# Optimization experiments

Hardware: AMD Instinct MI355X
Metric: run time of the kernel (lower is better)

## Reference

```python
import jax, jax.numpy as jnp
import numpy as np

SEQ, B, N, H, OUT, K, L = 32, 1024, 19, 128, 1, 2, 2


def setup_inputs() -> dict:
    key = jax.random.key(0)
    ks = jax.random.split(key, 16)
    s = lambda i, shape, scale=1.0: (jax.random.normal(ks[i], shape, jnp.float32) * scale)
    return {
        "inputs": s(0, (SEQ, B, N, OUT)),
        "initial_hidden_state": s(1, (L, B, N * H)),
        "support": s(2, (N, N)) * (1.0 / np.sqrt(N)),
        "W_gate0": s(3, (3 * (OUT + H), 2 * H)) * 0.05,
        "b_gate0": s(4, (2 * H,)) * 0.05,
        "W_cand0": s(5, (3 * (OUT + H), H)) * 0.05,
        "b_cand0": s(6, (H,)) * 0.05,
        "W_gate1": s(7, (3 * (H + H), 2 * H)) * 0.05,
        "b_gate1": s(8, (2 * H,)) * 0.05,
        "W_cand1": s(9, (3 * (H + H), H)) * 0.05,
        "b_cand1": s(10, (H,)) * 0.05,
        "W_proj": s(11, (H, OUT)) * 0.05,
        "b_proj": s(12, (OUT,)) * 0.05,
    }


def reference(inputs, initial_hidden_state, support, W_gate0, b_gate0, W_cand0,
              b_cand0, W_gate1, b_gate1, W_cand1, b_cand1, W_proj, b_proj):
    seq_len, batch = inputs.shape[0], inputs.shape[1]
    h0 = initial_hidden_state.reshape(L, batch, N, H)

    def gconv(x, W, b):
        # Chebyshev diffusion: x0, T1=S@x0, T2=2*S@T1-x0 (K=2, 1 support)
        x0 = x
        x1 = jnp.einsum('mn,bnf->bmf', support, x0)
        feats = [x0, x1]
        for _ in range(K - 1):
            x2 = 2.0 * jnp.einsum('mn,bnf->bmf', support, x1) - x0
            feats.append(x2)
            x0, x1 = x1, x2
        X = jnp.concatenate(feats, axis=-1)  # (B, N, F*num_matrices)
        return jnp.einsum('bnf,fo->bno', X, W) + b

    def cell(x_in, h, Wg, bg, Wc, bc):
        ru = jax.nn.sigmoid(gconv(jnp.concatenate([x_in, h], axis=-1), Wg, bg))
        r, u = jnp.split(ru, 2, axis=-1)
        c = jnp.tanh(gconv(jnp.concatenate([x_in, r * h], axis=-1), Wc, bc))
        return u * h + (1.0 - u) * c

    layer_params = [(W_gate0, b_gate0, W_cand0, b_cand0),
                    (W_gate1, b_gate1, W_cand1, b_cand1)]

    def step(carry, _):
        h, cur = carry
        new_h = []
        x = cur
        for i, (Wg, bg, Wc, bc) in enumerate(layer_params):
            x = cell(x, h[i], Wg, bg, Wc, bc)
            new_h.append(x)
        proj = jnp.einsum('bnh,ho->bno', x, W_proj) + b_proj  # (B, N, OUT)
        out_t = proj.reshape(batch, N * OUT)
        return (jnp.stack(new_h, axis=0), proj), out_t

    go = jnp.zeros((batch, N, OUT), inputs.dtype)
    (_, _), outputs = jax.lax.scan(step, (h0, go), None, length=seq_len)
    return outputs  # (seq_len, batch, N*OUT)
```

## Files before the change

kernel.cpp:

```cpp
#include <hip/hip_runtime.h>
#include <hip/hip_bf16.h>
#include <math.h>

#define SEQ   32
#define BATCH 1024
#define NN    19
#define HH    128
#define NB    4
#define MR    (NB*NN)
#define SAS   264
#define H0S   128
#define H1S   132
#define UBS   128
#define NBLK  (BATCH/NB)
#define NT    1024
#define UST_S 40

#define OFF_G0 0
#define OFF_C0 122880
#define OFF_G1 184320
#define OFF_C1 380928
#define WTOT   479232

#define OFF_H0  0
#define OFF_H1  19456
#define OFF_SA  59584
#define OFF_UB  101824
#define OFF_SBF 121280
#define OFF_UST 139712
#define OFF_XP  160192
#define LDS_BYTES 160496

__device__ unsigned short g_wall[WTOT];
__device__ unsigned short g_sbf[2*9*512];

typedef __attribute__((ext_vector_type(8))) short  bf16x8;
typedef __attribute__((ext_vector_type(4))) short  bf16x4;
typedef __attribute__((ext_vector_type(4))) float  f32x4;

__device__ __forceinline__ unsigned short f2bf(float v) {
    __hip_bfloat16 b = __float2bfloat16(v);
    return *reinterpret_cast<unsigned short*>(&b);
}
__device__ __forceinline__ float bf2f(unsigned short u) {
    unsigned int x = ((unsigned int)u) << 16;
    return __uint_as_float(x);
}
__device__ __forceinline__ float hload(const unsigned short* p) { return bf2f(*p); }
__device__ __forceinline__ float hload(const float* p)          { return *p; }
__device__ __forceinline__ void  hstore(unsigned short* p, float v) { *p = f2bf(v); }
__device__ __forceinline__ void  hstore(float* p, float v)          { *p = v; }

__global__ __launch_bounds__(256) void wconv_kernel(
    const float* __restrict__ W, int F, int O, int KP, int off, int l0)
{
    int idx = blockIdx.x*256 + threadIdx.x;
    int total = 3*O*KP;
    if (idx >= total) return;
    int j   = idx / (O*KP);
    int r   = idx - j*(O*KP);
    int col = r / KP;
    int k   = r - col*KP;
    int src;
    if (l0) src = (k < HH) ? k+1 : ((k == HH) ? 0 : -1);
    else    src = (k < F) ? k : -1;
    float v = (src >= 0) ? W[(size_t)(j*F + src)*O + col] : 0.f;
    g_wall[off + idx] = f2bf(v);
}

__global__ __launch_bounds__(256) void sbf_kernel(const float* __restrict__ S)
{
    __shared__ float sS[NN*NN], sS2[NN*NN];
    int tid = threadIdx.x;
    for (int i = tid; i < NN*NN; i += 256) sS[i] = S[i];
    __syncthreads();
    for (int i = tid; i < NN*NN; i += 256) {
        int m = i/NN, n = i - m*NN;
        float a = 0.f;
        for (int k = 0; k < NN; ++k) a += sS[m*NN+k]*sS[k*NN+n];
        sS2[i] = a;
    }
    __syncthreads();
    const int fmt[9] = {0,1,2, 1,2,3,4, 3,4};
    const int fkt[9] = {0,0,0, 1,1,1,1, 2,2};
    for (int idx = tid; idx < 2*9*512; idx += 256) {
        int mat = idx / 4608;
        int rem = idx - mat*4608;
        int i   = rem >> 9;
        int l   = (rem >> 3) & 63;
        int e   = rem & 7;
        int r   = fmt[i]*16 + (l & 15);
        int k   = fkt[i]*32 + (l >> 4)*8 + e;
        float v = 0.f;
        if (r < MR) {
            int b = r / NN, m = r - b*NN;
            int k0 = b*NN;
            if (k >= k0 && k < k0 + NN) {
                int n = k - k0;
                v = (mat == 0) ? sS[m*NN+n]
                               : (2.f*sS2[m*NN+n] - ((m==n)?1.f:0.f));
            }
        }
        g_sbf[idx] = f2bf(v);
    }
}

template<int KS, int OC, bool GATE, int XW, typename HT, int HSTR>
__device__ __forceinline__ void gconv_phase(
    const unsigned short* __restrict__ BT, const float* __restrict__ bias,
    HT* __restrict__ hL,
    unsigned short* __restrict__ sA, unsigned short* __restrict__ ub,
    const unsigned short* __restrict__ sbf, unsigned short* __restrict__ Ust,
    int lane, int w)
{
    constexpr int KP = KS*32;
    const int r16 = lane & 15, quad = lane >> 4;
    const int sgo = w*16;
    const bool act = (sgo < OC);

    constexpr int ktCnt[3]   = {3,4,2};
    constexpr int ktMT[3][4] = {{0,1,2,0},{1,2,3,4},{3,4,0,0}};
    constexpr int ktF0[3]    = {0,3,7};

    f32x4 acc[3][5];
    if (act) {
        const unsigned short* wb[3];
        #pragma unroll
        for (int j = 0; j < 3; ++j)
            wb[j] = BT + (size_t)(j*OC + sgo + r16)*KP + quad*8;

        #pragma unroll
        for (int j = 0; j < 3; ++j)
            #pragma unroll
            for (int mt = 0; mt < 5; ++mt) acc[j][mt] = (f32x4)0.f;

        bf16x8 ring[2][3];
        #pragma unroll
        for (int j = 0; j < 3; ++j) {
            ring[0][j] = *(const bf16x8*)(wb[j]);
            if (KS > 1) ring[1][j] = *(const bf16x8*)(wb[j] + 32);
        }
        #pragma unroll
        for (int ks = 0; ks < KS; ++ks) {
            bf16x8 bcur[3];
            #pragma unroll
            for (int j = 0; j < 3; ++j) bcur[j] = ring[ks & 1][j];
            if (ks + 2 < KS) {
                #pragma unroll
                for (int j = 0; j < 3; ++j)
                    ring[ks & 1][j] = *(const bf16x8*)(wb[j] + (ks + 2)*32);
            }
            #pragma unroll
            for (int mt = 0; mt < 5; ++mt) {
                bf16x8 af = *(const bf16x8*)&sA[(mt*16 + r16)*SAS + ks*32 + quad*8];
                #pragma unroll
                for (int j = 0; j < 3; ++j)
                    acc[j][mt] = __builtin_amdgcn_mfma_f32_16x16x32_bf16(
                        af, bcur[j], acc[j][mt], 0, 0, 0);
            }
        }

        #pragma unroll
        for (int jj = 1; jj <= 2; ++jj) {
            #pragma unroll
            for (int kt = 0; kt < 3; ++kt) {
                #pragma unroll
                for (int mtk = 0; mtk < 2; ++mtk) {
                    if (kt*2 + mtk < 5) {
                        bf16x4 pv;
                        pv[0] = (short)f2bf(acc[jj][kt*2+mtk][0]);
                        pv[1] = (short)f2bf(acc[jj][kt*2+mtk][1]);
                        pv[2] = (short)f2bf(acc[jj][kt*2+mtk][2]);
                        pv[3] = (short)f2bf(acc[jj][kt*2+mtk][3]);
                        *(bf16x4*)&Ust[r16*UST_S + mtk*16 + quad*4] = pv;
                    }
                }
                bf16x8 Bf = *(const bf16x8*)&Ust[r16*UST_S + quad*8];
                #pragma unroll
                for (int q = 0; q < ktCnt[kt]; ++q) {
                    const int mt = ktMT[kt][q];
                    bf16x8 af = *(const bf16x8*)
                        &sbf[((jj-1)*9 + ktF0[kt] + q)*512 + lane*8];
                    acc[0][mt] = __builtin_amdgcn_mfma_f32_16x16x32_bf16(
                        af, Bf, acc[0][mt], 0, 0, 0);
                }
            }
        }
    }

    float bv = act ? bias[sgo + r16] : 0.f;

    if (GATE) __syncthreads();

    if (act) {
        #pragma unroll
        for (int mt = 0; mt < 5; ++mt)
            #pragma unroll
            for (int reg = 0; reg < 4; ++reg) {
                int gm = mt*16 + quad*4 + reg;
                if (gm < MR) {
                    int o = sgo + r16;
                    float v = acc[0][mt][reg] + bv;
                    if (GATE) {
                        float sg_ = 1.f/(1.f + __expf(-v));
                        if (o < HH)
                            sA[gm*SAS + XW + o] =
                                f2bf(sg_ * hload(&hL[gm*HSTR + o]));
                        else
                            ub[gm*UBS + (o - HH)] = f2bf(sg_);
                    } else {
                        float c  = 2.f/(1.f + __expf(-2.f*v)) - 1.f;
                        float u  = bf2f(ub[gm*UBS + o]);
                        float ho = hload(&hL[gm*HSTR + o]);
                        hstore(&hL[gm*HSTR + o], u*ho + (1.f - u)*c);
                    }
                }
            }
    }
}

__global__ __launch_bounds__(NT)
__attribute__((amdgpu_waves_per_eu(4, 4)))
void dcgru_persistent(
    const float* __restrict__ ihs,
    const float* __restrict__ bg0, const float* __restrict__ bc0,
    const float* __restrict__ bg1, const float* __restrict__ bc1,
    const float* __restrict__ Wp, const float* __restrict__ bp,
    float* __restrict__ out)
{
    extern __shared__ char smem[];
    unsigned short* h0  = (unsigned short*)(smem + OFF_H0);
    float*          h1  = (float*)(smem + OFF_H1);
    unsigned short* sA  = (unsigned short*)(smem + OFF_SA);
    unsigned short* ub  = (unsigned short*)(smem + OFF_UB);
    unsigned short* sbf = (unsigned short*)(smem + OFF_SBF);
    float*       xprev  = (float*)(smem + OFF_XP);

    const int tid  = threadIdx.x;
    const int lane = tid & 63;
    const int w    = tid >> 6;
    const int bb   = blockIdx.x * NB;
    unsigned short* Ust = (unsigned short*)(smem + OFF_UST) + w*(16*UST_S);

    const unsigned short* BTg0 = g_wall + OFF_G0;
    const unsigned short* BTc0 = g_wall + OFF_C0;
    const unsigned short* BTg1 = g_wall + OFF_G1;
    const unsigned short* BTc1 = g_wall + OFF_C1;

    for (int i = tid; i < MR*HH; i += NT) {
        h0[i] = f2bf(ihs[(size_t)bb*2432 + i]);
        h1[(i >> 7)*H1S + (i & 127)] = ihs[(size_t)(BATCH + bb)*2432 + i];
    }
    for (int i = tid; i < MR; i += NT) xprev[i] = 0.f;
    for (int i = tid; i < 80*SAS/8; i += NT) ((bf16x8*)sA)[i] = (bf16x8)(short)0;
    for (int i = tid; i < 16*16*UST_S/8; i += NT)
        ((bf16x8*)(smem + OFF_UST))[i] = (bf16x8)(short)0;
    for (int i = tid; i < 2*9*512/8; i += NT)
        ((bf16x8*)sbf)[i] = ((const bf16x8*)g_sbf)[i];
    const float wp0 = Wp[lane], wp1 = Wp[64 + lane], bpv = bp[0];
    __syncthreads();

    for (int t = 0; t < SEQ; ++t) {
        for (int i = tid; i < MR*16; i += NT) {
            int row = i >> 4, ch = i & 15;
            *(bf16x8*)&sA[row*SAS + ch*8] =
                *(const bf16x8*)&h0[row*H0S + ch*8];
        }
        for (int i = tid; i < MR*4; i += NT) {
            int row = i >> 2, ch = i & 3;
            bf16x8 v = (bf16x8)(short)0;
            if (ch == 0) v[0] = (short)f2bf(xprev[row]);
            *(bf16x8*)&sA[row*SAS + HH + ch*8] = v;
        }
        __syncthreads();
        gconv_phase<5,256,true ,0,unsigned short,H0S>(BTg0, bg0, h0, sA, ub, sbf, Ust, lane, w);
        __syncthreads();
        gconv_phase<5,128,false,0,unsigned short,H0S>(BTc0, bc0, h0, sA, ub, sbf, Ust, lane, w);
        __syncthreads();

        for (int i = tid; i < MR*16; i += NT) {
            int row = i >> 4, ch = i & 15;
            *(bf16x8*)&sA[row*SAS + ch*8] =
                *(const bf16x8*)&h0[row*H0S + ch*8];
        }
        for (int i = tid; i < MR*16; i += NT) {
            int row = i >> 4, ch = i & 15;
            const float* hp = &h1[row*H1S + ch*8];
            f32x4 x0 = *(const f32x4*)hp;
            f32x4 x1 = *(const f32x4*)(hp + 4);
            bf16x8 v;
            v[0] = (short)f2bf(x0[0]); v[1] = (short)f2bf(x0[1]);
            v[2] = (short)f2bf(x0[2]); v[3] = (short)f2bf(x0[3]);
            v[4] = (short)f2bf(x1[0]); v[5] = (short)f2bf(x1[1]);
            v[6] = (short)f2bf(x1[2]); v[7] = (short)f2bf(x1[3]);
            *(bf16x8*)&sA[row*SAS + HH + ch*8] = v;
        }
        __syncthreads();
        gconv_phase<8,256,true ,HH,float,H1S>(BTg1, bg1, h1, sA, ub, sbf, Ust, lane, w);
        __syncthreads();
        gconv_phase<8,128,false,HH,float,H1S>(BTc1, bc1, h1, sA, ub, sbf, Ust, lane, w);
        __syncthreads();

        {
            int b  = w >> 2;
            int n0 = (w & 3) * 5;
            int n1 = n0 + 5; if (n1 > NN) n1 = NN;
            for (int n = n0; n < n1; ++n) {
                int row = b*NN + n;
                float s = h1[row*H1S + lane]*wp0 + h1[row*H1S + 64 + lane]*wp1;
                #pragma unroll
                for (int off = 32; off; off >>= 1) s += __shfl_down(s, off, 64);
                if (lane == 0) {
                    float v = s + bpv;
                    out[((size_t)t*BATCH + bb + b)*NN + n] = v;
                    xprev[row] = v;
                }
            }
        }
        __syncthreads();
    }
}

extern "C" void kernel_launch(void* const* d_in, const int* in_sizes, int n_in,
                              void* d_out, int out_size, void* d_ws, size_t ws_size,
                              hipStream_t stream) {
    const float* ihs = (const float*)d_in[1];
    const float* S   = (const float*)d_in[2];
    const float* Wg0 = (const float*)d_in[3];
    const float* bg0 = (const float*)d_in[4];
    const float* Wc0 = (const float*)d_in[5];
    const float* bc0 = (const float*)d_in[6];
    const float* Wg1 = (const float*)d_in[7];
    const float* bg1 = (const float*)d_in[8];
    const float* Wc1 = (const float*)d_in[9];
    const float* bc1 = (const float*)d_in[10];
    const float* Wp  = (const float*)d_in[11];
    const float* bp  = (const float*)d_in[12];
    float* out = (float*)d_out;

    sbf_kernel<<<1, 256, 0, stream>>>(S);
    wconv_kernel<<<(3*256*160+255)/256, 256, 0, stream>>>(Wg0, 129, 256, 160, OFF_G0, 1);
    wconv_kernel<<<(3*128*160+255)/256, 256, 0, stream>>>(Wc0, 129, 128, 160, OFF_C0, 1);
    wconv_kernel<<<(3*256*256+255)/256, 256, 0, stream>>>(Wg1, 256, 256, 256, OFF_G1, 0);
    wconv_kernel<<<(3*128*256+255)/256, 256, 0, stream>>>(Wc1, 256, 128, 256, OFF_C1, 0);

    hipFuncSetAttribute((const void*)dcgru_persistent,
                        hipFuncAttributeMaxDynamicSharedMemorySize, LDS_BYTES);

    dcgru_persistent<<<NBLK, NT, LDS_BYTES, stream>>>(
        ihs, bg0, bc0, bg1, bc1, Wp, bp, out);
}
```

Baseline: 2.361 ms.

## Halve batch per block and split gate GEMM into two passes over 8 waves

Each block now handles 2 batch elements (38 rows, padded to 48) with 512 threads instead of 4 elements with 1024 threads. The padded M dimension drops from 80 to 48, and the Chebyshev support tiles shrink from 9 to 5 per matrix, so less MFMA work goes to padding. LDS per block is roughly halved, which may allow two blocks per CU and doubles the grid size. The 256-wide gate output is split so each of the 8 waves runs two gcompute passes (u half, then r half), at the cost of reloading the A tiles and adding per-wave serial work.

```diff
diff --git a/kernel.cpp b/kernel.cpp
--- a/kernel.cpp
+++ b/kernel.cpp
@@ -6,14 +6,14 @@
 #define BATCH 1024
 #define NN    19
 #define HH    128
-#define NB    4
+#define NB    2
 #define MR    (NB*NN)
 #define SAS   264
 #define H0S   128
 #define H1S   132
 #define UBS   128
 #define NBLK  (BATCH/NB)
-#define NT    1024
+#define NT    512
 #define UST_S 40
 
 #define OFF_G0 0
@@ -23,16 +23,16 @@
 #define WTOT   479232
 
 #define OFF_H0  0
-#define OFF_H1  19456
-#define OFF_SA  59584
-#define OFF_UB  101824
-#define OFF_SBF 121280
-#define OFF_UST 139712
-#define OFF_XP  160192
-#define LDS_BYTES 160496
+#define OFF_H1  9728
+#define OFF_SA  29792
+#define OFF_UB  50912
+#define OFF_SBF 60640
+#define OFF_UST 70880
+#define OFF_XP  81120
+#define LDS_BYTES 81272
 
 __device__ unsigned short g_wall[WTOT];
-__device__ unsigned short g_sbf[2*9*512];
+__device__ unsigned short g_sbf[2*5*512];
 
 typedef __attribute__((ext_vector_type(8))) short  bf16x8;
 typedef __attribute__((ext_vector_type(4))) short  bf16x4;
@@ -46,10 +46,6 @@
     unsigned int x = ((unsigned int)u) << 16;
     return __uint_as_float(x);
 }
-__device__ __forceinline__ float hload(const unsigned short* p) { return bf2f(*p); }
-__device__ __forceinline__ float hload(const float* p)          { return *p; }
-__device__ __forceinline__ void  hstore(unsigned short* p, float v) { *p = f2bf(v); }
-__device__ __forceinline__ void  hstore(float* p, float v)          { *p = v; }
 
 __global__ __launch_bounds__(256) void wconv_kernel(
     const float* __restrict__ W, int F, int O, int KP, int off, int l0)
@@ -81,18 +77,18 @@
         sS2[i] = a;
     }
     __syncthreads();
-    const int fmt[9] = {0,1,2, 1,2,3,4, 3,4};
-    const int fkt[9] = {0,0,0, 1,1,1,1, 2,2};
-    for (int idx = tid; idx < 2*9*512; idx += 256) {
-        int mat = idx / 4608;
-        int rem = idx - mat*4608;
+    const int fmt[5] = {0,1,2, 1,2};
+    const int fkt[5] = {0,0,0, 1,1};
+    for (int idx = tid; idx < 2*5*512; idx += 256) {
+        int mat = idx / 2560;
+        int rem = idx - mat*2560;
         int i   = rem >> 9;
         int l   = (rem >> 3) & 63;
         int e   = rem & 7;
         int r   = fmt[i]*16 + (l & 15);
         int k   = fkt[i]*32 + (l >> 4)*8 + e;
         float v = 0.f;
-        if (r < MR) {
+        if (r < MR && k < MR) {
             int b = r / NN, m = r - b*NN;
             int k0 = b*NN;
             if (k >= k0 && k < k0 + NN) {
@@ -105,117 +101,82 @@
     }
 }
 
-template<int KS, int OC, bool GATE, int XW, typename HT, int HSTR>
-__device__ __forceinline__ void gconv_phase(
-    const unsigned short* __restrict__ BT, const float* __restrict__ bias,
-    HT* __restrict__ hL,
-    unsigned short* __restrict__ sA, unsigned short* __restrict__ ub,
-    const unsigned short* __restrict__ sbf, unsigned short* __restrict__ Ust,
-    int lane, int w)
+template<int KS, int OC>
+__device__ __forceinline__ void gcompute(
+    f32x4 (&acc)[3][3],
+    const unsigned short* __restrict__ BT,
+    const unsigned short* __restrict__ sA,
+    const unsigned short* __restrict__ sbf,
+    unsigned short* __restrict__ Ust,
+    int sgo, int lane)
 {
     constexpr int KP = KS*32;
     const int r16 = lane & 15, quad = lane >> 4;
-    const int sgo = w*16;
-    const bool act = (sgo < OC);
-
-    constexpr int ktCnt[3]   = {3,4,2};
-    constexpr int ktMT[3][4] = {{0,1,2,0},{1,2,3,4},{3,4,0,0}};
-    constexpr int ktF0[3]    = {0,3,7};
-
-    f32x4 acc[3][5];
-    if (act) {
-        const unsigned short* wb[3];
+
+    const unsigned short* wb[3];
+    #pragma unroll
+    for (int j = 0; j < 3; ++j)
+        wb[j] = BT + (size_t)(j*OC + sgo + r16)*KP + quad*8;
+
+    #pragma unroll
+    for (int j = 0; j < 3; ++j)
         #pragma unroll
-        for (int j = 0; j < 3; ++j)
-            wb[j] = BT + (size_t)(j*OC + sgo + r16)*KP + quad*8;
-
+        for (int mt = 0; mt < 3; ++mt) acc[j][mt] = (f32x4)0.f;
+
+    bf16x8 ring[2][3];
+    #pragma unroll
+    for (int j = 0; j < 3; ++j) {
+        ring[0][j] = *(const bf16x8*)(wb[j]);
+        if (KS > 1) ring[1][j] = *(const bf16x8*)(wb[j] + 32);
+    }
+    #pragma unroll
+    for (int ks = 0; ks < KS; ++ks) {
+        bf16x8 bcur[3];
         #pragma unroll
-        for (int j = 0; j < 3; ++j)
-            #pragma unroll
-            for (int mt = 0; mt < 5; ++mt) acc[j][mt] = (f32x4)0.f;
-
-        bf16x8 ring[2][3];
+        for (int j = 0; j < 3; ++j) bcur[j] = ring[ks & 1][j];
+        if (ks + 2 < KS) {
+            #pragma unroll
+            for (int j = 0; j < 3; ++j)
+                ring[ks & 1][j] = *(const bf16x8*)(wb[j] + (ks + 2)*32);
+        }
         #pragma unroll
-        for (int j = 0; j < 3; ++j) {
-            ring[0][j] = *(const bf16x8*)(wb[j]);
-            if (KS > 1) ring[1][j] = *(const bf16x8*)(wb[j] + 32);
-        }
+        for (int mt = 0; mt < 3; ++mt) {
+            bf16x8 af = *(const bf16x8*)&sA[(mt*16 + r16)*SAS + ks*32 + quad*8];
+            #pragma unroll
+            for (int j = 0; j < 3; ++j)
+                acc[j][mt] = __builtin_amdgcn_mfma_f32_16x16x32_bf16(
+                    af, bcur[j], acc[j][mt], 0, 0, 0);
+        }
+    }
+
+    constexpr int ktCnt[2]   = {3,2};
+    constexpr int ktMT[2][3] = {{0,1,2},{1,2,0}};
+    constexpr int ktF0[2]    = {0,3};
+    #pragma unroll
+    for (int jj = 1; jj <= 2; ++jj) {
         #pragma unroll
-        for (int ks = 0; ks < KS; ++ks) {
-            bf16x8 bcur[3];
-            #pragma unroll
-            for (int j = 0; j < 3; ++j) bcur[j] = ring[ks & 1][j];
-            if (ks + 2 < KS) {
-                #pragma unroll
-                for (int j = 0; j < 3; ++j)
-                    ring[ks & 1][j] = *(const bf16x8*)(wb[j] + (ks + 2)*32);
+        for (int kt = 0; kt < 2; ++kt) {
+            #pragma unroll
+            for (int mtk = 0; mtk < 2; ++mtk) {
+                if (kt*2 + mtk < 3) {
+                    bf16x4 pv;
+                    pv[0] = (short)f2bf(acc[jj][kt*2+mtk][0]);
+                    pv[1] = (short)f2bf(acc[jj][kt*2+mtk][1]);
+                    pv[2] = (short)f2bf(acc[jj][kt*2+mtk][2]);
+                    pv[3] = (short)f2bf(acc[jj][kt*2+mtk][3]);
+                    *(bf16x4*)&Ust[r16*UST_S + mtk*16 + quad*4] = pv;
+                }
             }
-            #pragma unroll
-            for (int mt = 0; mt < 5; ++mt) {
-                bf16x8 af = *(const bf16x8*)&sA[(mt*16 + r16)*SAS + ks*32 + quad*8];
-                #pragma unroll
-                for (int j = 0; j < 3; ++j)
-                    acc[j][mt] = __builtin_amdgcn_mfma_f32_16x16x32_bf16(
-                        af, bcur[j], acc[j][mt], 0, 0, 0);
+            bf16x8 Bf = *(const bf16x8*)&Ust[r16*UST_S + quad*8];
+            #pragma unroll
+            for (int q = 0; q < ktCnt[kt]; ++q) {
+                const int mt = ktMT[kt][q];
+                bf16x8 af = *(const bf16x8*)
+                    &sbf[((jj-1)*5 + ktF0[kt] + q)*512 + lane*8];
+                acc[0][mt] = __builtin_amdgcn_mfma_f32_16x16x32_bf16(
+                    af, Bf, acc[0][mt], 0, 0, 0);
             }
         }
-
-        #pragma unroll
-        for (int jj = 1; jj <= 2; ++jj) {
-            #pragma unroll
-            for (int kt = 0; kt < 3; ++kt) {
-                #pragma unroll
-                for (int mtk = 0; mtk < 2; ++mtk) {
-                    if (kt*2 + mtk < 5) {
-                        bf16x4 pv;
-                        pv[0] = (short)f2bf(acc[jj][kt*2+mtk][0]);
-                        pv[1] = (short)f2bf(acc[jj][kt*2+mtk][1]);
-                        pv[2] = (short)f2bf(acc[jj][kt*2+mtk][2]);
-                        pv[3] = (short)f2bf(acc[jj][kt*2+mtk][3]);
-                        *(bf16x4*)&Ust[r16*UST_S + mtk*16 + quad*4] = pv;
-                    }
-                }
-                bf16x8 Bf = *(const bf16x8*)&Ust[r16*UST_S + quad*8];
-                #pragma unroll
-                for (int q = 0; q < ktCnt[kt]; ++q) {
-                    const int mt = ktMT[kt][q];
-                    bf16x8 af = *(const bf16x8*)
-                        &sbf[((jj-1)*9 + ktF0[kt] + q)*512 + lane*8];
-                    acc[0][mt] = __builtin_amdgcn_mfma_f32_16x16x32_bf16(
-                        af, Bf, acc[0][mt], 0, 0, 0);
-                }
-            }
-        }
-    }
-
-    float bv = act ? bias[sgo + r16] : 0.f;
-
-    if (GATE) __syncthreads();
-
-    if (act) {
-        #pragma unroll
-        for (int mt = 0; mt < 5; ++mt)
-            #pragma unroll
-            for (int reg = 0; reg < 4; ++reg) {
-                int gm = mt*16 + quad*4 + reg;
-                if (gm < MR) {
-                    int o = sgo + r16;
-                    float v = acc[0][mt][reg] + bv;
-                    if (GATE) {
-                        float sg_ = 1.f/(1.f + __expf(-v));
-                        if (o < HH)
-                            sA[gm*SAS + XW + o] =
-                                f2bf(sg_ * hload(&hL[gm*HSTR + o]));
-                        else
-                            ub[gm*UBS + (o - HH)] = f2bf(sg_);
-                    } else {
-                        float c  = 2.f/(1.f + __expf(-2.f*v)) - 1.f;
-                        float u  = bf2f(ub[gm*UBS + o]);
-                        float ho = hload(&hL[gm*HSTR + o]);
-                        hstore(&hL[gm*HSTR + o], u*ho + (1.f - u)*c);
-                    }
-                }
-            }
     }
 }
 
@@ -239,6 +200,7 @@
     const int tid  = threadIdx.x;
     const int lane = tid & 63;
     const int w    = tid >> 6;
+    const int r16  = lane & 15, quad = lane >> 4;
     const int bb   = blockIdx.x * NB;
     unsigned short* Ust = (unsigned short*)(smem + OFF_UST) + w*(16*UST_S);
 
@@ -248,14 +210,15 @@
     const unsigned short* BTc1 = g_wall + OFF_C1;
 
     for (int i = tid; i < MR*HH; i += NT) {
-        h0[i] = f2bf(ihs[(size_t)bb*2432 + i]);
+        h0[(i >> 7)*H0S + (i & 127)] = f2bf(ihs[(size_t)bb*2432 + i]);
         h1[(i >> 7)*H1S + (i & 127)] = ihs[(size_t)(BATCH + bb)*2432 + i];
     }
     for (int i = tid; i < MR; i += NT) xprev[i] = 0.f;
-    for (int i = tid; i < 80*SAS/8; i += NT) ((bf16x8*)sA)[i] = (bf16x8)(short)0;
-    for (int i = tid; i < 16*16*UST_S/8; i += NT)
+    for (int i = tid; i < 40*SAS/8; i += NT) ((bf16x8*)sA)[i] = (bf16x8)(short)0;
+    for (int i = tid; i < MR*UBS/8; i += NT) ((bf16x8*)ub)[i] = (bf16x8)(short)0;
+    for (int i = tid; i < 8*16*UST_S/8; i += NT)
         ((bf16x8*)(smem + OFF_UST))[i] = (bf16x8)(short)0;
-    for (int i = tid; i < 2*9*512/8; i += NT)
+    for (int i = tid; i < 2*5*512/8; i += NT)
         ((bf16x8*)sbf)[i] = ((const bf16x8*)g_sbf)[i];
     const float wp0 = Wp[lane], wp1 = Wp[64 + lane], bpv = bp[0];
     __syncthreads();
@@ -273,9 +236,61 @@
             *(bf16x8*)&sA[row*SAS + HH + ch*8] = v;
         }
         __syncthreads();
-        gconv_phase<5,256,true ,0,unsigned short,H0S>(BTg0, bg0, h0, sA, ub, sbf, Ust, lane, w);
-        __syncthreads();
-        gconv_phase<5,128,false,0,unsigned short,H0S>(BTc0, bc0, h0, sA, ub, sbf, Ust, lane, w);
+
+        {
+            f32x4 a[3][3];
+            gcompute<5,256>(a, BTg0, sA, sbf, Ust, 128 + w*16, lane);
+            float bv = bg0[128 + w*16 + r16];
+            #pragma unroll
+            for (int mt = 0; mt < 3; ++mt)
+                #pragma unroll
+                for (int reg = 0; reg < 4; ++reg) {
+                    int gm = mt*16 + quad*4 + reg;
+                    if (gm < MR) {
+                        float v = a[0][mt][reg] + bv;
+                        ub[gm*UBS + w*16 + r16] = f2bf(1.f/(1.f + __expf(-v)));
+                    }
+                }
+        }
+        {
+            f32x4 a[3][3];
+            gcompute<5,256>(a, BTg0, sA, sbf, Ust, w*16, lane);
+            float bv = bg0[w*16 + r16];
+            __syncthreads();
+            #pragma unroll
+            for (int mt = 0; mt < 3; ++mt)
+                #pragma unroll
+                for (int reg = 0; reg < 4; ++reg) {
+                    int gm = mt*16 + quad*4 + reg;
+                    if (gm < MR) {
+                        int o = w*16 + r16;
+                        float v = a[0][mt][reg] + bv;
+                        float sg = 1.f/(1.f + __expf(-v));
+                        sA[gm*SAS + o] = f2bf(sg * bf2f(h0[gm*H0S + o]));
+                    }
+                }
+        }
+        __syncthreads();
+
+        {
+            f32x4 a[3][3];
+            gcompute<5,128>(a, BTc0, sA, sbf, Ust, w*16, lane);
+            float bv = bc0[w*16 + r16];
+            #pragma unroll
+            for (int mt = 0; mt < 3; ++mt)
+                #pragma unroll
+                for (int reg = 0; reg < 4; ++reg) {
+                    int gm = mt*16 + quad*4 + reg;
+                    if (gm < MR) {
+                        int o = w*16 + r16;
+                        float v = a[0][mt][reg] + bv;
+                        float c = 2.f/(1.f + __expf(-2.f*v)) - 1.f;
+                        float u = bf2f(ub[gm*UBS + o]);
+                        float ho = bf2f(h0[gm*H0S + o]);
+                        h0[gm*H0S + o] = f2bf(u*ho + (1.f - u)*c);
+                    }
+                }
+        }
         __syncthreads();
 
         for (int i = tid; i < MR*16; i += NT) {
@@ -296,24 +311,74 @@
             *(bf16x8*)&sA[row*SAS + HH + ch*8] = v;
         }
         __syncthreads();
-        gconv_phase<8,256,true ,HH,float,H1S>(BTg1, bg1, h1, sA, ub, sbf, Ust, lane, w);
-        __syncthreads();
-        gconv_phase<8,128,false,HH,float,H1S>(BTc1, bc1, h1, sA, ub, sbf, Ust, lane, w);
-        __syncthreads();
-
-        {
-            int b  = w >> 2;
-            int n0 = (w & 3) * 5;
-            int n1 = n0 + 5; if (n1 > NN) n1 = NN;
-            for (int n = n0; n < n1; ++n) {
-                int row = b*NN + n;
-                float s = h1[row*H1S + lane]*wp0 + h1[row*H1S + 64 + lane]*wp1;
+
+        {
+            f32x4 a[3][3];
+            gcompute<8,256>(a, BTg1, sA, sbf, Ust, 128 + w*16, lane);
+            float bv = bg1[128 + w*16 + r16];
+            #pragma unroll
+            for (int mt = 0; mt < 3; ++mt)
+                #pragma unroll
+                for (int reg = 0; reg < 4; ++reg) {
+                    int gm = mt*16 + quad*4 + reg;
+                    if (gm < MR) {
+                        float v = a[0][mt][reg] + bv;
+                        ub[gm*UBS + w*16 + r16] = f2bf(1.f/(1.f + __expf(-v)));
+                    }
+                }
+        }
+        {
+            f32x4 a[3][3];
+            gcompute<8,256>(a, BTg1, sA, sbf, Ust, w*16, lane);
+            float bv = bg1[w*16 + r16];
+            __syncthreads();
+            #pragma unroll
+            for (int mt = 0; mt < 3; ++mt)
+                #pragma unroll
+                for (int reg = 0; reg < 4; ++reg) {
+                    int gm = mt*16 + quad*4 + reg;
+                    if (gm < MR) {
+                        int o = w*16 + r16;
+                        float v = a[0][mt][reg] + bv;
+                        float sg = 1.f/(1.f + __expf(-v));
+                        sA[gm*SAS + HH + o] = f2bf(sg * h1[gm*H1S + o]);
+                    }
+                }
+        }
+        __syncthreads();
+
+        {
+            f32x4 a[3][3];
+            gcompute<8,128>(a, BTc1, sA, sbf, Ust, w*16, lane);
+            float bv = bc1[w*16 + r16];
+            #pragma unroll
+            for (int mt = 0; mt < 3; ++mt)
+                #pragma unroll
+                for (int reg = 0; reg < 4; ++reg) {
+                    int gm = mt*16 + quad*4 + reg;
+                    if (gm < MR) {
+                        int o = w*16 + r16;
+                        float v = a[0][mt][reg] + bv;
+                        float c = 2.f/(1.f + __expf(-2.f*v)) - 1.f;
+                        float u = bf2f(ub[gm*UBS + o]);
+                        float ho = h1[gm*H1S + o];
+                        h1[gm*H1S + o] = u*ho + (1.f - u)*c;
+                    }
+                }
+        }
+        __syncthreads();
+
+        {
+            int rA = w*5;
+            for (int rr = rA; rr < rA + 5 && rr < MR; ++rr) {
+                int b = rr / NN, n = rr - b*NN;
+                float s = h1[rr*H1S + lane]*wp0 + h1[rr*H1S + 64 + lane]*wp1;
                 #pragma unroll
                 for (int off = 32; off; off >>= 1) s += __shfl_down(s, off, 64);
                 if (lane == 0) {
                     float v = s + bpv;
                     out[((size_t)t*BATCH + bb + b)*NN + n] = v;
-                    xprev[row] = v;
+                    xprev[rr] = v;
                 }
             }
         }
```

Result: slower. 2.412 ms (+2.2%).

## Apply layer-0 scalar input as rank-1 FMA and keep h0 resident in LDS

Applied to the files above, without the earlier changes.

Layer 0's single input feature was padded to a full 32-wide K slice of the MFMA loop. It is now dropped from the GEMM (KS 5→4) and added as a rank-1 update: the x value times a per-column weight read from a new g_wx table, applied to each diffusion slot's accumulator before the Chebyshev mixing. The candidate phase also writes the updated h0 straight into sA, so the per-timestep reload of h0 and xprev into LDS goes away and the block needs fewer barriers. In exchange it adds an extra __syncthreads in the layer-0 candidate phase, scalar FMAs per accumulator, and xprev/g_wx global reads.

```diff
diff --git a/kernel.cpp b/kernel.cpp
--- a/kernel.cpp
+++ b/kernel.cpp
@@ -17,10 +17,10 @@
 #define UST_S 40
 
 #define OFF_G0 0
-#define OFF_C0 122880
-#define OFF_G1 184320
-#define OFF_C1 380928
-#define WTOT   479232
+#define OFF_C0 98304
+#define OFF_G1 147456
+#define OFF_C1 344064
+#define WTOT   442368
 
 #define OFF_H0  0
 #define OFF_H1  19456
@@ -32,6 +32,7 @@
 #define LDS_BYTES 160496
 
 __device__ unsigned short g_wall[WTOT];
+__device__ float g_wx[3*256 + 3*128];
 __device__ unsigned short g_sbf[2*9*512];
 
 typedef __attribute__((ext_vector_type(8))) short  bf16x8;
@@ -62,10 +63,24 @@
     int col = r / KP;
     int k   = r - col*KP;
     int src;
-    if (l0) src = (k < HH) ? k+1 : ((k == HH) ? 0 : -1);
+    if (l0) src = k + 1;
     else    src = (k < F) ? k : -1;
-    float v = (src >= 0) ? W[(size_t)(j*F + src)*O + col] : 0.f;
+    float v = (src >= 0 && src < F) ? W[(size_t)(j*F + src)*O + col] : 0.f;
     g_wall[off + idx] = f2bf(v);
+}
+
+__global__ __launch_bounds__(256) void wx_kernel(
+    const float* __restrict__ Wg0, const float* __restrict__ Wc0)
+{
+    int i = blockIdx.x*256 + threadIdx.x;
+    if (i < 3*256) {
+        int j = i >> 8, col = i & 255;
+        g_wx[i] = Wg0[(size_t)(j*129)*256 + col];
+    } else if (i < 3*256 + 3*128) {
+        int r = i - 3*256;
+        int j = r >> 7, col = r & 127;
+        g_wx[i] = Wc0[(size_t)(j*129)*128 + col];
+    }
 }
 
 __global__ __launch_bounds__(256) void sbf_kernel(const float* __restrict__ S)
@@ -105,12 +120,14 @@
     }
 }
 
-template<int KS, int OC, bool GATE, int XW, typename HT, int HSTR>
+template<int KS, int OC, bool GATE, int XW, bool X1, bool WS,
+         typename HT, int HSTR>
 __device__ __forceinline__ void gconv_phase(
     const unsigned short* __restrict__ BT, const float* __restrict__ bias,
     HT* __restrict__ hL,
     unsigned short* __restrict__ sA, unsigned short* __restrict__ ub,
     const unsigned short* __restrict__ sbf, unsigned short* __restrict__ Ust,
+    const float* __restrict__ wx, const float* __restrict__ xprev,
     int lane, int w)
 {
     constexpr int KP = KS*32;
@@ -158,6 +175,22 @@
                     acc[j][mt] = __builtin_amdgcn_mfma_f32_16x16x32_bf16(
                         af, bcur[j], acc[j][mt], 0, 0, 0);
             }
+        }
+
+        if (X1) {
+            float wxv[3];
+            #pragma unroll
+            for (int j = 0; j < 3; ++j) wxv[j] = wx[j*OC + sgo + r16];
+            #pragma unroll
+            for (int mt = 0; mt < 5; ++mt)
+                #pragma unroll
+                for (int reg = 0; reg < 4; ++reg) {
+                    int gm = mt*16 + quad*4 + reg;
+                    float xv = (gm < MR) ? xprev[gm] : 0.f;
+                    #pragma unroll
+                    for (int j = 0; j < 3; ++j)
+                        acc[j][mt][reg] += xv * wxv[j];
+                }
         }
 
         #pragma unroll
@@ -190,7 +223,7 @@
 
     float bv = act ? bias[sgo + r16] : 0.f;
 
-    if (GATE) __syncthreads();
+    if (GATE || WS) __syncthreads();
 
     if (act) {
         #pragma unroll
@@ -212,7 +245,9 @@
                         float c  = 2.f/(1.f + __expf(-2.f*v)) - 1.f;
                         float u  = bf2f(ub[gm*UBS + o]);
                         float ho = hload(&hL[gm*HSTR + o]);
-                        hstore(&hL[gm*HSTR + o], u*ho + (1.f - u)*c);
+                        float hn = u*ho + (1.f - u)*c;
+                        hstore(&hL[gm*HSTR + o], hn);
+                        if (WS) sA[gm*SAS + o] = f2bf(hn);
                     }
                 }
             }
@@ -259,30 +294,20 @@
         ((bf16x8*)sbf)[i] = ((const bf16x8*)g_sbf)[i];
     const float wp0 = Wp[lane], wp1 = Wp[64 + lane], bpv = bp[0];
     __syncthreads();
+    for (int i = tid; i < MR*16; i += NT) {
+        int row = i >> 4, ch = i & 15;
+        *(bf16x8*)&sA[row*SAS + ch*8] = *(const bf16x8*)&h0[row*H0S + ch*8];
+    }
+    __syncthreads();
 
     for (int t = 0; t < SEQ; ++t) {
-        for (int i = tid; i < MR*16; i += NT) {
-            int row = i >> 4, ch = i & 15;
-            *(bf16x8*)&sA[row*SAS + ch*8] =
-                *(const bf16x8*)&h0[row*H0S + ch*8];
-        }
-        for (int i = tid; i < MR*4; i += NT) {
-            int row = i >> 2, ch = i & 3;
-            bf16x8 v = (bf16x8)(short)0;
-            if (ch == 0) v[0] = (short)f2bf(xprev[row]);
-            *(bf16x8*)&sA[row*SAS + HH + ch*8] = v;
-        }
-        __syncthreads();
-        gconv_phase<5,256,true ,0,unsigned short,H0S>(BTg0, bg0, h0, sA, ub, sbf, Ust, lane, w);
-        __syncthreads();
-        gconv_phase<5,128,false,0,unsigned short,H0S>(BTc0, bc0, h0, sA, ub, sbf, Ust, lane, w);
-        __syncthreads();
-
-        for (int i = tid; i < MR*16; i += NT) {
-            int row = i >> 4, ch = i & 15;
-            *(bf16x8*)&sA[row*SAS + ch*8] =
-                *(const bf16x8*)&h0[row*H0S + ch*8];
-        }
+        gconv_phase<4,256,true ,0,true ,false,unsigned short,H0S>(
+            BTg0, bg0, h0, sA, ub, sbf, Ust, g_wx, xprev, lane, w);
+        __syncthreads();
+        gconv_phase<4,128,false,0,true ,true ,unsigned short,H0S>(
+            BTc0, bc0, h0, sA, ub, sbf, Ust, g_wx + 3*256, xprev, lane, w);
+        __syncthreads();
+
         for (int i = tid; i < MR*16; i += NT) {
             int row = i >> 4, ch = i & 15;
             const float* hp = &h1[row*H1S + ch*8];
@@ -296,9 +321,11 @@
             *(bf16x8*)&sA[row*SAS + HH + ch*8] = v;
         }
         __syncthreads();
-        gconv_phase<8,256,true ,HH,float,H1S>(BTg1, bg1, h1, sA, ub, sbf, Ust, lane, w);
-        __syncthreads();
-        gconv_phase<8,128,false,HH,float,H1S>(BTc1, bc1, h1, sA, ub, sbf, Ust, lane, w);
+        gconv_phase<8,256,true ,HH,false,false,float,H1S>(
+            BTg1, bg1, h1, sA, ub, sbf, Ust, nullptr, xprev, lane, w);
+        __syncthreads();
+        gconv_phase<8,128,false,HH,false,false,float,H1S>(
+            BTc1, bc1, h1, sA, ub, sbf, Ust, nullptr, xprev, lane, w);
         __syncthreads();
 
         {
@@ -339,8 +366,9 @@
     float* out = (float*)d_out;
 
     sbf_kernel<<<1, 256, 0, stream>>>(S);
-    wconv_kernel<<<(3*256*160+255)/256, 256, 0, stream>>>(Wg0, 129, 256, 160, OFF_G0, 1);
-    wconv_kernel<<<(3*128*160+255)/256, 256, 0, stream>>>(Wc0, 129, 128, 160, OFF_C0, 1);
+    wx_kernel<<<5, 256, 0, stream>>>(Wg0, Wc0);
+    wconv_kernel<<<(3*256*128+255)/256, 256, 0, stream>>>(Wg0, 129, 256, 128, OFF_G0, 1);
+    wconv_kernel<<<(3*128*128+255)/256, 256, 0, stream>>>(Wc0, 129, 128, 128, OFF_C0, 1);
     wconv_kernel<<<(3*256*256+255)/256, 256, 0, stream>>>(Wg1, 256, 256, 256, OFF_G1, 0);
     wconv_kernel<<<(3*128*256+255)/256, 256, 0, stream>>>(Wc1, 256, 128, 256, OFF_C1, 0);
 
```

New measurement: 2.801 ms. 1.19x slower.
